# Optimization experiments

Hardware: AMD Instinct MI355X
Metric: run time of the kernel (lower is better)

The kernel has to match this reference:

```python
import jax, jax.numpy as jnp
import numpy as np
from jax import lax

B, N, K, M, NC = 64, 1024, 20, 256, 40  # clouds, points/cloud, knn k, fps points (ratio 0.25), classes
EPS = 1e-5


def setup_inputs() -> dict:
    key = jax.random.key(0)
    ks = jax.random.split(key, 6)
    w = lambda k, s: jax.random.normal(k, s, jnp.float32) * 0.05
    return {
        "pos": jax.random.normal(ks[0], (B * N, 3), jnp.float32),
        "w1": w(ks[1], (64, 3)), "b1": jnp.zeros(64, jnp.float32),
        "g1": jnp.ones(64, jnp.float32), "be1": jnp.zeros(64, jnp.float32),
        "w2": w(ks[2], (64, 64)), "b2": jnp.zeros(64, jnp.float32),
        "g2": jnp.ones(64, jnp.float32), "be2": jnp.zeros(64, jnp.float32),
        "w_nn1": w(ks[3], (512, 64)), "b_nn1": jnp.zeros(512, jnp.float32),
        "g_bn2": jnp.ones(512, jnp.float32), "be_bn2": jnp.zeros(512, jnp.float32),
        "w_nn4": w(ks[4], (NC, 512)), "b_nn4": jnp.zeros(NC, jnp.float32),
    }


def _knn_idx(p):  # p: [N,3] -> [N,K] neighbor indices, self excluded (loop=False)
    d = jnp.sum(p * p, -1)[:, None] + jnp.sum(p * p, -1)[None, :] - 2.0 * (p @ p.T)
    d = d.at[jnp.arange(N), jnp.arange(N)].set(jnp.inf)
    _, idx = lax.top_k(-d, K)
    return idx


def _fps_idx(p):  # p: [N,3] -> [M] farthest-point-sampling indices (deterministic start at 0)
    def step(carry, _):
        dist, last = carry
        d = jnp.sum((p - p[last]) ** 2, -1)
        dist = jnp.minimum(dist, d)
        nxt = jnp.argmax(dist).astype(jnp.int32)
        return (dist, nxt), nxt
    init = (jnp.full((N,), 1e38, jnp.float32), jnp.int32(0))
    _, idxs = lax.scan(step, init, None, length=M - 1)
    return jnp.concatenate([jnp.zeros((1,), jnp.int32), idxs])


def _bn(x, g, b, axes):  # batch-norm with batch statistics (training mode)
    m = jnp.mean(x, axes, keepdims=True)
    v = jnp.var(x, axes, keepdims=True)
    return (x - m) * lax.rsqrt(v + EPS) * g + b


def reference(pos, w1, b1, g1, be1, w2, b2, g2, be2,
              w_nn1, b_nn1, g_bn2, be_bn2, w_nn4, b_nn4):
    p = pos.reshape(B, N, 3)
    idx = jax.vmap(_knn_idx)(p)                     # [B,N,K]
    nbr = jax.vmap(lambda pb, ib: pb[ib])(p, idx)   # [B,N,K,3]
    rel = nbr - p[:, :, None, :]                    # edge features (relative positions)
    h = jax.nn.relu(jnp.einsum('bnkc,fc->bnkf', rel, w1) + b1)
    h = _bn(h, g1, be1, (0, 1, 2))
    h = jax.nn.relu(jnp.einsum('bnkf,gf->bnkg', h, w2) + b2)
    h = _bn(h, g2, be2, (0, 1, 2))
    feat = jnp.max(h, axis=2)                       # [B,N,64] edge-conv max aggregation
    fidx = jax.vmap(_fps_idx)(p)                    # [B,M]
    f = jnp.take_along_axis(feat, fidx[:, :, None], axis=1)  # [B,M,64]
    y = jnp.einsum('bmf,hf->bmh', f, w_nn1) + b_nn1  # [B,M,512]
    y = jnp.max(y, axis=1)                           # [B,512]
    y = jax.nn.relu(y)
    y = _bn(y, g_bn2, be_bn2, (0,))
    y = y @ w_nn4.T + b_nn4                          # [B,40]
    return jax.nn.log_softmax(y, axis=1)
```

## Files before the change

kernel.cpp:

```cpp
#include <hip/hip_runtime.h>
#include <hip/hip_bf16.h>
#include <cfloat>
#include <math.h>

#define BB 64
#define NN 1024
#define KNN 20
#define MM 256
#define CC 64
#define HH 512
#define NCLS 40
#define EPSF 1e-5f
#define CNT1 (BB*NN*KNN)

#define FPS_R1 101
#define FPS_R2 151

#define IDX_OFF    0
#define MAXH2_OFF  (IDX_OFF + BB*NN*KNN)
#define FIDX_OFF   (MAXH2_OFF + BB*NN*CC)
#define Y_OFF      (FIDX_OFF + BB*MM)
#define ACC_OFF    (Y_OFF + BB*HH)
#define W2T_OFF    (ACC_OFF + 256)
#define B2F_OFF    (W2T_OFF + CC*CC)
#define S2_OFF     (B2F_OFF + CC)
#define T2_OFF     (S2_OFF + CC)
#define S3_OFF     (T2_OFF + CC)
#define T3_OFF     (S3_OFF + HH)
#define FPSD_OFF   (T3_OFF + HH)
#define FPSC_OFF   (FPSD_OFF + BB*NN)

typedef __attribute__((ext_vector_type(8)))  short short8;
typedef __attribute__((ext_vector_type(16))) float f32x16;

static __device__ __forceinline__ unsigned short f2bf(float f) {
  unsigned u = __float_as_uint(f);
  unsigned r = (u + 0x7fffu + ((u >> 16) & 1u)) >> 16;
  return (unsigned short)r;
}

static __device__ __forceinline__ void fps_phase(
    const float* sx, const float* sy, const float* sz,
    float* fpsd, int* fpsc, int* fidxg, int b, int mStart, int mEnd) {
  int lane = threadIdx.x;
  float lx[16], ly[16], lz[16], dist[16];
#pragma unroll
  for (int q = 0; q < 16; ++q) {
    int j = q*64 + lane;
    lx[q] = sx[j]; ly[q] = sy[j]; lz[q] = sz[j];
  }
  int cur;
  if (mStart <= 1) {
#pragma unroll
    for (int q = 0; q < 16; ++q) dist[q] = 1e38f;
    if (lane == 0) fidxg[b*MM] = 0;
    cur = 0;
  } else {
#pragma unroll
    for (int q = 0; q < 16; ++q) dist[q] = fpsd[b*NN + q*64 + lane];
    cur = fpsc[b];
  }
  for (int m = mStart; m < mEnd; ++m) {
    float cpx = sx[cur], cpy = sy[cur], cpz = sz[cur];
#pragma unroll
    for (int q = 0; q < 16; ++q) {
      float dx = __fsub_rn(lx[q], cpx);
      float dy = __fsub_rn(ly[q], cpy);
      float dz = __fsub_rn(lz[q], cpz);
      float dd = __fadd_rn(__fadd_rn(__fmul_rn(dx,dx), __fmul_rn(dy,dy)), __fmul_rn(dz,dz));
      dist[q] = fminf(dist[q], dd);
    }
    float t8[8];
#pragma unroll
    for (int q = 0; q < 8; ++q) t8[q] = fmaxf(dist[q], dist[q + 8]);
#pragma unroll
    for (int q = 0; q < 4; ++q) t8[q] = fmaxf(t8[q], t8[q + 4]);
    float r = fmaxf(fmaxf(t8[0], t8[1]), fmaxf(t8[2], t8[3]));
#define FPS_VMAX_STEP(C) { \
    int tt = __builtin_amdgcn_update_dpp(__float_as_int(r), __float_as_int(r), (C), 0xf, 0xf, false); \
    r = fmaxf(r, __int_as_float(tt)); }
    FPS_VMAX_STEP(0x111)
    FPS_VMAX_STEP(0x112)
    FPS_VMAX_STEP(0x114)
    FPS_VMAX_STEP(0x118)
    FPS_VMAX_STEP(0x142)
    FPS_VMAX_STEP(0x143)
#undef FPS_VMAX_STEP
    float wmax = __int_as_float(__builtin_amdgcn_readlane(__float_as_int(r), 63));
    unsigned ci = 0xFFFFFFFFu;
#pragma unroll
    for (int q = 15; q >= 0; --q)
      if (dist[q] == wmax) ci = (unsigned)(q*64 + lane);
#define FPS_IMIN_STEP(C) { \
    unsigned tt = (unsigned)__builtin_amdgcn_update_dpp((int)ci, (int)ci, (C), 0xf, 0xf, false); \
    ci = (tt < ci) ? tt : ci; }
    FPS_IMIN_STEP(0x111)
    FPS_IMIN_STEP(0x112)
    FPS_IMIN_STEP(0x114)
    FPS_IMIN_STEP(0x118)
    FPS_IMIN_STEP(0x142)
    FPS_IMIN_STEP(0x143)
#undef FPS_IMIN_STEP
    cur = (int)(unsigned)__builtin_amdgcn_readlane((int)ci, 63);
    if (lane == 0) fidxg[b*MM + m] = cur;
  }
  if (mEnd < MM) {
#pragma unroll
    for (int q = 0; q < 16; ++q) fpsd[b*NN + q*64 + lane] = dist[q];
    if (lane == 0) fpsc[b] = cur;
  }
}

__global__ __launch_bounds__(256) void knn_fps_kernel(const float* __restrict__ pos,
                                                      int* __restrict__ idxg,
                                                      int* __restrict__ fidxg,
                                                      float* __restrict__ fpsd,
                                                      int* __restrict__ fpsc) {
  __shared__ float4 pj[NN];
  if (blockIdx.x >= BB) {
    int blk = blockIdx.x - BB;
    int b  = blk >> 5;
    int nb = blk & 31;
    const float* pb = pos + (size_t)b * NN * 3;
    for (int i = threadIdx.x; i < NN; i += 256) {
      float x = pb[i*3+0], y = pb[i*3+1], z = pb[i*3+2];
      pj[i] = make_float4(x, y, z, (x*x + y*y) + z*z);
    }
    __syncthreads();
    int lane = threadIdx.x & 63;
    int wv   = threadIdx.x >> 6;
    unsigned long long lmask_lt = (1ULL << lane) - 1ULL;

    for (int t = 0; t < 8; ++t) {
      int i = nb*32 + wv*8 + t;
      float4 pi = pj[i];
      unsigned u[16];
#pragma unroll
      for (int q = 0; q < 16; ++q) {
        int j = q*64 + lane;
        float4 pw = pj[j];
        float d = pi.w + pw.w - 2.0f*(pi.x*pw.x + pi.y*pw.y + pi.z*pw.z);
        unsigned bits = __float_as_uint(d);
        bits = (bits & 0x80000000u) ? ~bits : (bits | 0x80000000u);
        if (j == i) bits = 0xFFFFFFFFu;
        u[q] = bits;
      }
      unsigned lmin = u[0];
#pragma unroll
      for (int q = 1; q < 16; ++q) lmin = (u[q] < lmin) ? u[q] : lmin;
      unsigned rmin = lmin, rmax = lmin;
#define KNN_DPP_STEP(C) { \
      unsigned t1 = (unsigned)__builtin_amdgcn_update_dpp((int)rmin, (int)rmin, (C), 0xf, 0xf, false); \
      unsigned t2 = (unsigned)__builtin_amdgcn_update_dpp((int)rmax, (int)rmax, (C), 0xf, 0xf, false); \
      rmin = (t1 < rmin) ? t1 : rmin; rmax = (t2 > rmax) ? t2 : rmax; }
      KNN_DPP_STEP(0x111)
      KNN_DPP_STEP(0x112)
      KNN_DPP_STEP(0x114)
      KNN_DPP_STEP(0x118)
      KNN_DPP_STEP(0x142)
      KNN_DPP_STEP(0x143)
#undef KNN_DPP_STEP
      unsigned plo = ((unsigned)__builtin_amdgcn_readlane((int)rmin, 63)) >> 16;
      unsigned phi = ((unsigned)__builtin_amdgcn_readlane((int)rmax, 63)) >> 16;
      int cntHi = -1;
      while (plo < phi) {
        unsigned pmid = (plo + phi) >> 1;
        unsigned tmid = (pmid << 16) | 0xFFFFu;
        int cnt = 0;
#pragma unroll
        for (int q = 0; q < 16; ++q)
          cnt += (int)__popcll(__ballot(u[q] <= tmid));
        if (cnt >= KNN) { phi = pmid; cntHi = cnt; } else plo = pmid + 1;
      }
      unsigned tstar = (phi << 16) | 0xFFFFu;
      unsigned bbase = phi << 16;
      int* op = idxg + (size_t)(b*NN + i) * KNN;
      if (cntHi < 0) {
        cntHi = 0;
#pragma unroll
        for (int q = 0; q < 16; ++q)
          cntHi += (int)__popcll(__ballot(u[q] <= tstar));
      }
      if (cntHi == KNN) {
        int base = 0;
#pragma unroll
        for (int q = 0; q < 16; ++q) {
          bool pred = (u[q] <= tstar);
          unsigned long long mask = __ballot((int)pred);
          if (pred) op[base + (int)__popcll(mask & lmask_lt)] = q*64 + lane;
          base += (int)__popcll(mask);
        }
      } else {
        unsigned lo2 = bbase, hi2 = tstar;
        while (lo2 < hi2) {
          unsigned mid = lo2 + ((hi2 - lo2) >> 1);
          int cnt = 0;
#pragma unroll
          for (int q = 0; q < 16; ++q)
            cnt += (int)__popcll(__ballot(u[q] <= mid));
          if (cnt >= KNN) hi2 = mid; else lo2 = mid + 1;
        }
        unsigned xstar = lo2;
        int base = 0;
#pragma unroll
        for (int q = 0; q < 16; ++q) {
          bool pred = (u[q] < xstar);
          unsigned long long mask = __ballot((int)pred);
          if (pred) op[base + (int)__popcll(mask & lmask_lt)] = q*64 + lane;
          base += (int)__popcll(mask);
        }
        for (int q = 0; q < 16 && base < KNN; ++q) {
          bool pred = (u[q] == xstar);
          unsigned long long mask = __ballot((int)pred);
          if (pred) {
            int pos_ = base + (int)__popcll(mask & lmask_lt);
            if (pos_ < KNN) op[pos_] = q*64 + lane;
          }
          base += (int)__popcll(mask);
        }
      }
    }
  } else {
    int b = blockIdx.x;
    float* base = (float*)pj;
    float* sx = base; float* sy = base + NN; float* sz = base + 2*NN;
    const float* pb = pos + (size_t)b * NN * 3;
    for (int i = threadIdx.x; i < NN; i += 256) {
      sx[i] = pb[i*3+0]; sy[i] = pb[i*3+1]; sz[i] = pb[i*3+2];
    }
    __syncthreads();
    if (threadIdx.x >= 64) return;
    fps_phase(sx, sy, sz, fpsd, fpsc, fidxg, b, 1, FPS_R1);
  }
}

__global__ __launch_bounds__(256) void stats1_kernel(const float* __restrict__ pos,
    const int* __restrict__ idxg, const float* __restrict__ w1,
    const float* __restrict__ b1, float* __restrict__ acc,
    int* __restrict__ fidxg, float* __restrict__ fpsd, int* __restrict__ fpsc) {
  __shared__ float px[NN], py[NN], pz[NN];
  __shared__ float relx[4][KNN], rely[4][KNN], relz[4][KNN];
  __shared__ float red[4][CC];
  if (blockIdx.x < BB) {
    int b = blockIdx.x;
    const float* pb = pos + (size_t)b*NN*3;
    for (int i = threadIdx.x; i < NN; i += 256) {
      px[i] = pb[i*3+0]; py[i] = pb[i*3+1]; pz[i] = pb[i*3+2];
    }
    __syncthreads();
    if (threadIdx.x >= 64) return;
    fps_phase(px, py, pz, fpsd, fpsc, fidxg, b, FPS_R1, FPS_R2);
    return;
  }
  int blk = blockIdx.x - BB;
  int b = blk >> 4;
  int nb = blk & 15;
  const float* pb = pos + (size_t)b*NN*3;
  for (int i = threadIdx.x; i < NN; i += 256) {
    px[i] = pb[i*3+0]; py[i] = pb[i*3+1]; pz[i] = pb[i*3+2];
  }
  int c = threadIdx.x & 63, w = threadIdx.x >> 6;
  float w1x = w1[c*3+0], w1y = w1[c*3+1], w1z = w1[c*3+2], b1c = b1[c];
  float s = 0.f, ss = 0.f;
  __syncthreads();
  for (int it = 0; it < 16; ++it) {
    int n0 = nb*64 + it*4;
    if (threadIdx.x < 80) {
      int wv = threadIdx.x / KNN, k = threadIdx.x % KNN;
      int n = n0 + wv;
      int j = idxg[(size_t)(b*NN + n)*KNN + k];
      relx[wv][k] = px[j] - px[n];
      rely[wv][k] = py[j] - py[n];
      relz[wv][k] = pz[j] - pz[n];
    }
    __syncthreads();
#pragma unroll
    for (int k = 0; k < KNN; ++k) {
      float h = fmaxf(relx[w][k]*w1x + rely[w][k]*w1y + relz[w][k]*w1z + b1c, 0.f);
      s += h; ss += h*h;
    }
    __syncthreads();
  }
  red[w][c] = s; __syncthreads();
  if (w == 0) atomicAdd(&acc[c], red[0][c]+red[1][c]+red[2][c]+red[3][c]);
  __syncthreads();
  red[w][c] = ss; __syncthreads();
  if (w == 0) atomicAdd(&acc[64+c], red[0][c]+red[1][c]+red[2][c]+red[3][c]);
}

__global__ void fold1_kernel(const float* __restrict__ acc, const float* __restrict__ g1,
    const float* __restrict__ be1, const float* __restrict__ w2, const float* __restrict__ b2,
    unsigned short* __restrict__ w2bf, float* __restrict__ b2f) {
  __shared__ float s1[CC], t1[CC];
  int tid = threadIdx.x;
  if (tid < CC) {
    float cnt = (float)CNT1;
    float m = acc[tid] / cnt;
    float v = acc[64+tid] / cnt - m*m;
    float sc = g1[tid] * rsqrtf(v + EPSF);
    s1[tid] = sc; t1[tid] = be1[tid] - m*sc;
  }
  __syncthreads();
  int frag = tid >> 6;
  int lane = tid & 63;
  int nt = frag >> 2, ks = frag & 3;
  int cout = nt*32 + (lane & 31);
  int cin0 = ks*16 + (lane >> 5)*8;
  for (int j = 0; j < 8; ++j) {
    int cin = cin0 + j;
    w2bf[((size_t)frag*64 + lane)*8 + j] = f2bf(w2[cout*CC + cin] * s1[cin]);
  }
  if (tid < CC) {
    float accb = b2[tid];
    for (int ci = 0; ci < CC; ++ci) accb += t1[ci]*w2[tid*CC + ci];
    b2f[tid] = accb;
  }
}

__global__ __launch_bounds__(256, 4) void conv2_kernel(const float* __restrict__ pos,
    const int* __restrict__ idxg, const float* __restrict__ w1, const float* __restrict__ b1,
    const unsigned short* __restrict__ w2bf, const float* __restrict__ b2fg,
    float* __restrict__ maxh2, float* __restrict__ acc2,
    int* __restrict__ fidxg, float* __restrict__ fpsd, int* __restrict__ fpsc) {
  __shared__ float px[NN], py[NN], pz[NN];
  __shared__ float4 relw[4][KNN];
  __shared__ __align__(16) unsigned short h1s[4][2112];
  __shared__ float redbuf[4][2*CC];
  if (blockIdx.x < BB) {
    int b = blockIdx.x;
    const float* pb = pos + (size_t)b*NN*3;
    for (int i = threadIdx.x; i < NN; i += 256) {
      px[i] = pb[i*3+0]; py[i] = pb[i*3+1]; pz[i] = pb[i*3+2];
    }
    __syncthreads();
    if (threadIdx.x >= 64) return;
    fps_phase(px, py, pz, fpsd, fpsc, fidxg, b, FPS_R2, MM);
    return;
  }
  int blk = blockIdx.x - BB;
  int b = blk >> 4;
  int nb = blk & 15;
  const float* pb = pos + (size_t)b*NN*3;
  for (int i = threadIdx.x; i < NN; i += 256) {
    px[i] = pb[i*3+0]; py[i] = pb[i*3+1]; pz[i] = pb[i*3+2];
  }
  int lane = threadIdx.x & 63, w = threadIdx.x >> 6;
  int half = lane >> 5, l31 = lane & 31;
  short8 Bf[2][4];
#pragma unroll
  for (int nt = 0; nt < 2; ++nt)
#pragma unroll
    for (int ks = 0; ks < 4; ++ks)
      Bf[nt][ks] = *(const short8*)&w2bf[((size_t)(nt*4+ks)*64 + lane)*8];
  float b2o0 = b2fg[l31], b2o1 = b2fg[32 + l31];
  float w1x = w1[lane*3+0], w1y = w1[lane*3+1], w1z = w1[lane*3+2], b1c = b1[lane];
  unsigned short* hw = h1s[w];
  {
    short8 zz = {0,0,0,0,0,0,0,0};
    for (int z = lane; z < 96; z += 64) {
      int g = z / 12, r = 20 + z % 12;
      *(short8*)&hw[g*264 + r*8] = zz;
    }
  }
  float sA = 0.f, ssA = 0.f, sB = 0.f, ssB = 0.f;
  __syncthreads();
  for (int t = 0; t < 16; ++t) {
    int n = nb*64 + w*16 + t;
    if (lane < KNN) {
      int j = idxg[(size_t)(b*NN + n)*KNN + lane];
      relw[w][lane] = make_float4(px[j]-px[n], py[j]-py[n], pz[j]-pz[n], 0.f);
    }
    int gbase = (lane >> 3)*264 + (lane & 7);
#pragma unroll
    for (int k = 0; k < KNN; ++k) {
      float4 r4 = relw[w][k];
      float h = fmaxf(fmaf(r4.x, w1x, fmaf(r4.y, w1y, fmaf(r4.z, w1z, b1c))), 0.f);
      hw[gbase + k*8] = f2bf(h);
    }
    f32x16 acc0 = {}; f32x16 acc1 = {};
#pragma unroll
    for (int ks = 0; ks < 4; ++ks) {
      short8 A = *(const short8*)&hw[(ks*2 + half)*264 + l31*8];
      acc0 = __builtin_amdgcn_mfma_f32_32x32x16_bf16(A, Bf[0][ks], acc0, 0, 0, 0);
      acc1 = __builtin_amdgcn_mfma_f32_32x32x16_bf16(A, Bf[1][ks], acc1, 0, 0, 0);
    }
    float mx0 = 0.f, mx1 = 0.f;
#pragma unroll
    for (int reg = 0; reg < 8; ++reg) {
      float v0 = fmaxf(acc0[reg] + b2o0, 0.f);
      float v1 = fmaxf(acc1[reg] + b2o1, 0.f);
      sA += v0; ssA += v0*v0; sB += v1; ssB += v1*v1;
      mx0 = fmaxf(mx0, v0); mx1 = fmaxf(mx1, v1);
    }
    if (half == 0) {
#pragma unroll
      for (int reg = 8; reg < 12; ++reg) {
        float v0 = fmaxf(acc0[reg] + b2o0, 0.f);
        float v1 = fmaxf(acc1[reg] + b2o1, 0.f);
        sA += v0; ssA += v0*v0; sB += v1; ssB += v1*v1;
        mx0 = fmaxf(mx0, v0); mx1 = fmaxf(mx1, v1);
      }
    }
    mx0 = fmaxf(mx0, __shfl_xor(mx0, 32, 64));
    mx1 = fmaxf(mx1, __shfl_xor(mx1, 32, 64));
    if (half == 0) {
      float* mp = maxh2 + (size_t)(b*NN + n)*CC;
      mp[l31] = mx0; mp[32 + l31] = mx1;
    }
  }
  sA += __shfl_xor(sA, 32, 64); ssA += __shfl_xor(ssA, 32, 64);
  sB += __shfl_xor(sB, 32, 64); ssB += __shfl_xor(ssB, 32, 64);
  if (half == 0) { redbuf[w][l31] = sA; redbuf[w][32 + l31] = sB; }
  __syncthreads();
  if (w == 0) atomicAdd(&acc2[lane], redbuf[0][lane]+redbuf[1][lane]+redbuf[2][lane]+redbuf[3][lane]);
  __syncthreads();
  if (half == 0) { redbuf[w][l31] = ssA; redbuf[w][32 + l31] = ssB; }
  __syncthreads();
  if (w == 0) atomicAdd(&acc2[64+lane], redbuf[0][lane]+redbuf[1][lane]+redbuf[2][lane]+redbuf[3][lane]);
}

__global__ void fold2_kernel(const float* __restrict__ acc2, const float* __restrict__ g2,
    const float* __restrict__ be2, float* __restrict__ s2, float* __restrict__ t2) {
  int c = threadIdx.x;
  float cnt = (float)CNT1;
  float m = acc2[c]/cnt;
  float v = acc2[64+c]/cnt - m*m;
  float sc = g2[c]*rsqrtf(v+EPSF);
  s2[c] = sc;
  t2[c] = be2[c] - m*sc;
}

__global__ __launch_bounds__(256) void head_kernel(const float* __restrict__ maxh2,
    const int* __restrict__ fidxg, const float* __restrict__ s2g, const float* __restrict__ t2g,
    const float* __restrict__ wnn1, const float* __restrict__ bnn1, float* __restrict__ Y) {
  int b = blockIdx.x >> 2;
  int hc = blockIdx.x & 3;
  __shared__ __align__(16) float ftile[128][CC];
  __shared__ float red2[4][128];
  int hl = threadIdx.x & 63, mseg = threadIdx.x >> 6;
  int hA = hc*128 + hl, hB = hA + 64;
  float4 wva[16], wvb[16];
  const float4* wrA = (const float4*)(wnn1 + (size_t)hA*CC);
  const float4* wrB = (const float4*)(wnn1 + (size_t)hB*CC);
#pragma unroll
  for (int q = 0; q < 16; ++q) { wva[q] = wrA[q]; wvb[q] = wrB[q]; }
  float bestA = -FLT_MAX, bestB = -FLT_MAX;
  const int* fb = fidxg + b*MM;
  for (int chunk = 0; chunk < 2; ++chunk) {
    {
      int row = threadIdx.x & 127, chal = threadIdx.x >> 7;
      int fi = fb[chunk*128 + row];
      const float* src = maxh2 + (size_t)(b*NN + fi)*CC;
      for (int ci = chal*32; ci < chal*32+32; ++ci)
        ftile[row][ci] = s2g[ci]*src[ci] + t2g[ci];
    }
    __syncthreads();
    for (int m = mseg*32; m < mseg*32+32; ++m) {
      float accA = 0.f, accB = 0.f;
#pragma unroll
      for (int cq = 0; cq < 16; ++cq) {
        float4 f = *((const float4*)&ftile[m][cq*4]);
        accA = fmaf(f.x, wva[cq].x, accA);
        accA = fmaf(f.y, wva[cq].y, accA);
        accA = fmaf(f.z, wva[cq].z, accA);
        accA = fmaf(f.w, wva[cq].w, accA);
        accB = fmaf(f.x, wvb[cq].x, accB);
        accB = fmaf(f.y, wvb[cq].y, accB);
        accB = fmaf(f.z, wvb[cq].z, accB);
        accB = fmaf(f.w, wvb[cq].w, accB);
      }
      bestA = fmaxf(bestA, accA);
      bestB = fmaxf(bestB, accB);
    }
    __syncthreads();
  }
  red2[mseg][hl] = bestA;
  red2[mseg][64 + hl] = bestB;
  __syncthreads();
  if (threadIdx.x < 128) {
    int hh = hc*128 + threadIdx.x;
    float v = fmaxf(fmaxf(red2[0][threadIdx.x], red2[1][threadIdx.x]),
                    fmaxf(red2[2][threadIdx.x], red2[3][threadIdx.x])) + bnn1[hh];
    Y[(size_t)b*HH + hh] = fmaxf(v, 0.f);
  }
}

__global__ void bn3_kernel(const float* __restrict__ Y, const float* __restrict__ g,
    const float* __restrict__ be, float* __restrict__ s3, float* __restrict__ t3) {
  int h = blockIdx.x*256 + threadIdx.x;
  float s = 0.f;
  for (int b = 0; b < BB; ++b) s += Y[(size_t)b*HH + h];
  float m = s / (float)BB;
  float v = 0.f;
  for (int b = 0; b < BB; ++b) { float d = Y[(size_t)b*HH + h] - m; v += d*d; }
  v /= (float)BB;
  float sc = g[h] * rsqrtf(v + EPSF);
  s3[h] = sc; t3[h] = be[h] - m*sc;
}

__global__ __launch_bounds__(256) void logits_kernel(const float* __restrict__ Y,
    const float* __restrict__ s3, const float* __restrict__ t3,
    const float* __restrict__ w4, const float* __restrict__ b4, float* __restrict__ out) {
  int b = blockIdx.x;
  __shared__ float ybn[HH];
  __shared__ float lg[NCLS];
  __shared__ float lse;
  for (int hh = threadIdx.x; hh < HH; hh += 256)
    ybn[hh] = Y[(size_t)b*HH + hh]*s3[hh] + t3[hh];
  __syncthreads();
  if (threadIdx.x < NCLS) {
    int j = threadIdx.x;
    float acc = b4[j];
    const float* wr = w4 + (size_t)j*HH;
    for (int ci = 0; ci < HH; ++ci) acc = fmaf(ybn[ci], wr[ci], acc);
    lg[j] = acc;
  }
  __syncthreads();
  if (threadIdx.x == 0) {
    float mx = -FLT_MAX;
    for (int j = 0; j < NCLS; ++j) mx = fmaxf(mx, lg[j]);
    float s = 0.f;
    for (int j = 0; j < NCLS; ++j) s += expf(lg[j] - mx);
    lse = mx + logf(s);
  }
  __syncthreads();
  if (threadIdx.x < NCLS) out[b*NCLS + threadIdx.x] = lg[threadIdx.x] - lse;
}

extern "C" void kernel_launch(void* const* d_in, const int* in_sizes, int n_in,
                              void* d_out, int out_size, void* d_ws, size_t ws_size,
                              hipStream_t stream) {
  const float* pos  = (const float*)d_in[0];
  const float* w1   = (const float*)d_in[1];
  const float* b1   = (const float*)d_in[2];
  const float* g1   = (const float*)d_in[3];
  const float* be1  = (const float*)d_in[4];
  const float* w2   = (const float*)d_in[5];
  const float* b2   = (const float*)d_in[6];
  const float* g2   = (const float*)d_in[7];
  const float* be2  = (const float*)d_in[8];
  const float* wnn1 = (const float*)d_in[9];
  const float* bnn1 = (const float*)d_in[10];
  const float* gbn2 = (const float*)d_in[11];
  const float* bebn2= (const float*)d_in[12];
  const float* wnn4 = (const float*)d_in[13];
  const float* bnn4 = (const float*)d_in[14];
  float* ws = (float*)d_ws;
  int*   idxg  = (int*)(ws + IDX_OFF);
  float* maxh2 = ws + MAXH2_OFF;
  int*   fidxg = (int*)(ws + FIDX_OFF);
  float* Y     = ws + Y_OFF;
  float* acc1  = ws + ACC_OFF;
  float* acc2  = ws + ACC_OFF + 128;
  unsigned short* w2bf = (unsigned short*)(ws + W2T_OFF);
  float* b2f   = ws + B2F_OFF;
  float* s2    = ws + S2_OFF;
  float* t2    = ws + T2_OFF;
  float* s3    = ws + S3_OFF;
  float* t3    = ws + T3_OFF;
  float* fpsd  = ws + FPSD_OFF;
  int*   fpsc  = (int*)(ws + FPSC_OFF);
  float* outp  = (float*)d_out;

  hipMemsetAsync((void*)(ws + ACC_OFF), 0, 256*sizeof(float), stream);
  knn_fps_kernel<<<BB + BB*32, 256, 0, stream>>>(pos, idxg, fidxg, fpsd, fpsc);
  stats1_kernel<<<BB + BB*16, 256, 0, stream>>>(pos, idxg, w1, b1, acc1, fidxg, fpsd, fpsc);
  fold1_kernel<<<1, 512, 0, stream>>>(acc1, g1, be1, w2, b2, w2bf, b2f);
  conv2_kernel<<<BB + BB*16, 256, 0, stream>>>(pos, idxg, w1, b1, w2bf, b2f, maxh2, acc2, fidxg, fpsd, fpsc);
  fold2_kernel<<<1, 64, 0, stream>>>(acc2, g2, be2, s2, t2);
  head_kernel<<<BB*4, 256, 0, stream>>>(maxh2, fidxg, s2, t2, wnn1, bnn1, Y);
  bn3_kernel<<<2, 256, 0, stream>>>(Y, gbn2, bebn2, s3, t3);
  logits_kernel<<<BB, 256, 0, stream>>>(Y, s3, t3, wnn4, bnn4, outp);
}
```

Before: 371.4 us.

## Process two KNN query points per wave iteration and rebalance FPS split

The KNN selection loop now handles two query points at once. Their distance computation, DPP reductions and radix-threshold binary searches are interleaved so the serial ballot/popcount chains overlap for instruction-level parallelism. Lane prefix counts now use mbcnt instead of a mask-and-popcount, and the FPS phase boundaries are moved so more iterations run inside the concurrent KNN kernel. The interleaved search runs until both points converge, so one point may do wasted iterations, and register pressure rises.

```diff
diff --git a/kernel.cpp b/kernel.cpp
--- a/kernel.cpp
+++ b/kernel.cpp
@@ -13,8 +13,8 @@
 #define EPSF 1e-5f
 #define CNT1 (BB*NN*KNN)
 
-#define FPS_R1 101
-#define FPS_R2 151
+#define FPS_R1 131
+#define FPS_R2 176
 
 #define IDX_OFF    0
 #define MAXH2_OFF  (IDX_OFF + BB*NN*KNN)
@@ -37,6 +37,55 @@
   unsigned u = __float_as_uint(f);
   unsigned r = (u + 0x7fffu + ((u >> 16) & 1u)) >> 16;
   return (unsigned short)r;
+}
+
+static __device__ __forceinline__ int mbcnt64(unsigned long long m) {
+  return (int)__builtin_amdgcn_mbcnt_hi((unsigned)(m >> 32),
+           __builtin_amdgcn_mbcnt_lo((unsigned)m, 0));
+}
+
+static __device__ __forceinline__ void knn_emit_generic(const unsigned* u, unsigned phi,
+                                                        int cntHi, int* op, int lane) {
+  unsigned tstar = (phi << 16) | 0xFFFFu;
+  unsigned bbase = phi << 16;
+  if (cntHi == KNN) {
+    int base = 0;
+#pragma unroll
+    for (int q = 0; q < 16; ++q) {
+      bool pred = (u[q] <= tstar);
+      unsigned long long mask = __ballot((int)pred);
+      if (pred) op[base + mbcnt64(mask)] = q*64 + lane;
+      base += (int)__popcll(mask);
+    }
+  } else {
+    unsigned lo2 = bbase, hi2 = tstar;
+    while (lo2 < hi2) {
+      unsigned mid = lo2 + ((hi2 - lo2) >> 1);
+      int cnt = 0;
+#pragma unroll
+      for (int q = 0; q < 16; ++q)
+        cnt += (int)__popcll(__ballot(u[q] <= mid));
+      if (cnt >= KNN) hi2 = mid; else lo2 = mid + 1;
+    }
+    unsigned xstar = lo2;
+    int base = 0;
+#pragma unroll
+    for (int q = 0; q < 16; ++q) {
+      bool pred = (u[q] < xstar);
+      unsigned long long mask = __ballot((int)pred);
+      if (pred) op[base + mbcnt64(mask)] = q*64 + lane;
+      base += (int)__popcll(mask);
+    }
+    for (int q = 0; q < 16 && base < KNN; ++q) {
+      bool pred = (u[q] == xstar);
+      unsigned long long mask = __ballot((int)pred);
+      if (pred) {
+        int pos_ = base + mbcnt64(mask);
+        if (pos_ < KNN) op[pos_] = q*64 + lane;
+      }
+      base += (int)__popcll(mask);
+    }
+  }
 }
 
 static __device__ __forceinline__ void fps_phase(
@@ -129,30 +178,42 @@
     __syncthreads();
     int lane = threadIdx.x & 63;
     int wv   = threadIdx.x >> 6;
-    unsigned long long lmask_lt = (1ULL << lane) - 1ULL;
-
-    for (int t = 0; t < 8; ++t) {
-      int i = nb*32 + wv*8 + t;
-      float4 pi = pj[i];
-      unsigned u[16];
+
+    for (int t = 0; t < 4; ++t) {
+      int iA = nb*32 + wv*8 + 2*t;
+      int iB = iA + 1;
+      float4 piA = pj[iA];
+      float4 piB = pj[iB];
+      unsigned uA[16], uB[16];
 #pragma unroll
       for (int q = 0; q < 16; ++q) {
         int j = q*64 + lane;
         float4 pw = pj[j];
-        float d = pi.w + pw.w - 2.0f*(pi.x*pw.x + pi.y*pw.y + pi.z*pw.z);
-        unsigned bits = __float_as_uint(d);
-        bits = (bits & 0x80000000u) ? ~bits : (bits | 0x80000000u);
-        if (j == i) bits = 0xFFFFFFFFu;
-        u[q] = bits;
-      }
-      unsigned lmin = u[0];
-#pragma unroll
-      for (int q = 1; q < 16; ++q) lmin = (u[q] < lmin) ? u[q] : lmin;
-      unsigned rmin = lmin, rmax = lmin;
+        float dA = piA.w + pw.w - 2.0f*(piA.x*pw.x + piA.y*pw.y + piA.z*pw.z);
+        float dB = piB.w + pw.w - 2.0f*(piB.x*pw.x + piB.y*pw.y + piB.z*pw.z);
+        unsigned ba = __float_as_uint(dA);
+        ba = (ba & 0x80000000u) ? ~ba : (ba | 0x80000000u);
+        if (j == iA) ba = 0xFFFFFFFFu;
+        uA[q] = ba;
+        unsigned bb2 = __float_as_uint(dB);
+        bb2 = (bb2 & 0x80000000u) ? ~bb2 : (bb2 | 0x80000000u);
+        if (j == iB) bb2 = 0xFFFFFFFFu;
+        uB[q] = bb2;
+      }
+      unsigned lminA = uA[0], lminB = uB[0];
+#pragma unroll
+      for (int q = 1; q < 16; ++q) {
+        lminA = (uA[q] < lminA) ? uA[q] : lminA;
+        lminB = (uB[q] < lminB) ? uB[q] : lminB;
+      }
+      unsigned rminA = lminA, rmaxA = lminA, rminB = lminB, rmaxB = lminB;
 #define KNN_DPP_STEP(C) { \
-      unsigned t1 = (unsigned)__builtin_amdgcn_update_dpp((int)rmin, (int)rmin, (C), 0xf, 0xf, false); \
-      unsigned t2 = (unsigned)__builtin_amdgcn_update_dpp((int)rmax, (int)rmax, (C), 0xf, 0xf, false); \
-      rmin = (t1 < rmin) ? t1 : rmin; rmax = (t2 > rmax) ? t2 : rmax; }
+      unsigned t1 = (unsigned)__builtin_amdgcn_update_dpp((int)rminA, (int)rminA, (C), 0xf, 0xf, false); \
+      unsigned t2 = (unsigned)__builtin_amdgcn_update_dpp((int)rmaxA, (int)rmaxA, (C), 0xf, 0xf, false); \
+      unsigned t3 = (unsigned)__builtin_amdgcn_update_dpp((int)rminB, (int)rminB, (C), 0xf, 0xf, false); \
+      unsigned t4 = (unsigned)__builtin_amdgcn_update_dpp((int)rmaxB, (int)rmaxB, (C), 0xf, 0xf, false); \
+      rminA = (t1 < rminA) ? t1 : rminA; rmaxA = (t2 > rmaxA) ? t2 : rmaxA; \
+      rminB = (t3 < rminB) ? t3 : rminB; rmaxB = (t4 > rmaxB) ? t4 : rmaxB; }
       KNN_DPP_STEP(0x111)
       KNN_DPP_STEP(0x112)
       KNN_DPP_STEP(0x114)
@@ -160,64 +221,53 @@
       KNN_DPP_STEP(0x142)
       KNN_DPP_STEP(0x143)
 #undef KNN_DPP_STEP
-      unsigned plo = ((unsigned)__builtin_amdgcn_readlane((int)rmin, 63)) >> 16;
-      unsigned phi = ((unsigned)__builtin_amdgcn_readlane((int)rmax, 63)) >> 16;
-      int cntHi = -1;
-      while (plo < phi) {
-        unsigned pmid = (plo + phi) >> 1;
-        unsigned tmid = (pmid << 16) | 0xFFFFu;
-        int cnt = 0;
-#pragma unroll
-        for (int q = 0; q < 16; ++q)
-          cnt += (int)__popcll(__ballot(u[q] <= tmid));
-        if (cnt >= KNN) { phi = pmid; cntHi = cnt; } else plo = pmid + 1;
-      }
-      unsigned tstar = (phi << 16) | 0xFFFFu;
-      unsigned bbase = phi << 16;
-      int* op = idxg + (size_t)(b*NN + i) * KNN;
-      if (cntHi < 0) {
-        cntHi = 0;
-#pragma unroll
-        for (int q = 0; q < 16; ++q)
-          cntHi += (int)__popcll(__ballot(u[q] <= tstar));
-      }
-      if (cntHi == KNN) {
-        int base = 0;
+      unsigned ploA = ((unsigned)__builtin_amdgcn_readlane((int)rminA, 63)) >> 16;
+      unsigned phiA = ((unsigned)__builtin_amdgcn_readlane((int)rmaxA, 63)) >> 16;
+      unsigned ploB = ((unsigned)__builtin_amdgcn_readlane((int)rminB, 63)) >> 16;
+      unsigned phiB = ((unsigned)__builtin_amdgcn_readlane((int)rmaxB, 63)) >> 16;
+      int cntHiA = -1, cntHiB = -1;
+      while (ploA < phiA || ploB < phiB) {
+        unsigned pmA = (ploA + phiA) >> 1, pmB = (ploB + phiB) >> 1;
+        unsigned tA = (pmA << 16) | 0xFFFFu, tB = (pmB << 16) | 0xFFFFu;
+        int cA = 0, cB = 0;
 #pragma unroll
         for (int q = 0; q < 16; ++q) {
-          bool pred = (u[q] <= tstar);
-          unsigned long long mask = __ballot((int)pred);
-          if (pred) op[base + (int)__popcll(mask & lmask_lt)] = q*64 + lane;
-          base += (int)__popcll(mask);
+          cA += (int)__popcll(__ballot(uA[q] <= tA));
+          cB += (int)__popcll(__ballot(uB[q] <= tB));
+        }
+        if (ploA < phiA) { if (cA >= KNN) { phiA = pmA; cntHiA = cA; } else ploA = pmA + 1; }
+        if (ploB < phiB) { if (cB >= KNN) { phiB = pmB; cntHiB = cB; } else ploB = pmB + 1; }
+      }
+      if (cntHiA < 0 || cntHiB < 0) {
+        unsigned tsA = (phiA << 16) | 0xFFFFu, tsB = (phiB << 16) | 0xFFFFu;
+        int cA = 0, cB = 0;
+#pragma unroll
+        for (int q = 0; q < 16; ++q) {
+          cA += (int)__popcll(__ballot(uA[q] <= tsA));
+          cB += (int)__popcll(__ballot(uB[q] <= tsB));
+        }
+        if (cntHiA < 0) cntHiA = cA;
+        if (cntHiB < 0) cntHiB = cB;
+      }
+      int* opA = idxg + (size_t)(b*NN + iA) * KNN;
+      int* opB = idxg + (size_t)(b*NN + iB) * KNN;
+      if (cntHiA == KNN && cntHiB == KNN) {
+        unsigned tsA = (phiA << 16) | 0xFFFFu, tsB = (phiB << 16) | 0xFFFFu;
+        int baseA = 0, baseB = 0;
+#pragma unroll
+        for (int q = 0; q < 16; ++q) {
+          bool pA = (uA[q] <= tsA);
+          unsigned long long mA = __ballot((int)pA);
+          bool pB = (uB[q] <= tsB);
+          unsigned long long mB = __ballot((int)pB);
+          if (pA) opA[baseA + mbcnt64(mA)] = q*64 + lane;
+          if (pB) opB[baseB + mbcnt64(mB)] = q*64 + lane;
+          baseA += (int)__popcll(mA);
+          baseB += (int)__popcll(mB);
         }
       } else {
-        unsigned lo2 = bbase, hi2 = tstar;
-        while (lo2 < hi2) {
-          unsigned mid = lo2 + ((hi2 - lo2) >> 1);
-          int cnt = 0;
-#pragma unroll
-          for (int q = 0; q < 16; ++q)
-            cnt += (int)__popcll(__ballot(u[q] <= mid));
-          if (cnt >= KNN) hi2 = mid; else lo2 = mid + 1;
-        }
-        unsigned xstar = lo2;
-        int base = 0;
-#pragma unroll
-        for (int q = 0; q < 16; ++q) {
-          bool pred = (u[q] < xstar);
-          unsigned long long mask = __ballot((int)pred);
-          if (pred) op[base + (int)__popcll(mask & lmask_lt)] = q*64 + lane;
-          base += (int)__popcll(mask);
-        }
-        for (int q = 0; q < 16 && base < KNN; ++q) {
-          bool pred = (u[q] == xstar);
-          unsigned long long mask = __ballot((int)pred);
-          if (pred) {
-            int pos_ = base + (int)__popcll(mask & lmask_lt);
-            if (pos_ < KNN) op[pos_] = q*64 + lane;
-          }
-          base += (int)__popcll(mask);
-        }
+        knn_emit_generic(uA, phiA, cntHiA, opA, lane);
+        knn_emit_generic(uB, phiB, cntHiB, opB, lane);
       }
     }
   } else {
```

Measured after the change: 409.1 us. 1.1x slower.

## Fuse BN fold kernels into head and logits kernels, rebalance FPS phase split

Applied to the files above, without the earlier changes.

Removes the separate fold2 and bn3 launches. Each head block now recomputes the BN2 scale and shift into shared memory, and each logits block recomputes the BN3 batch statistics redundantly. This removes two tiny kernel launches and their serialization gaps. The FPS phase boundaries (how the sampling steps are split across the knn, stats and conv kernels) also move later, shifting work between the fused kernels. The cost is redundant per-block reduction work: every one of the 64 logits blocks rereads all of Y.

```diff
diff --git a/kernel.cpp b/kernel.cpp
--- a/kernel.cpp
+++ b/kernel.cpp
@@ -13,8 +13,8 @@
 #define EPSF 1e-5f
 #define CNT1 (BB*NN*KNN)
 
-#define FPS_R1 101
-#define FPS_R2 151
+#define FPS_R1 131
+#define FPS_R2 176
 
 #define IDX_OFF    0
 #define MAXH2_OFF  (IDX_OFF + BB*NN*KNN)
@@ -23,11 +23,7 @@
 #define ACC_OFF    (Y_OFF + BB*HH)
 #define W2T_OFF    (ACC_OFF + 256)
 #define B2F_OFF    (W2T_OFF + CC*CC)
-#define S2_OFF     (B2F_OFF + CC)
-#define T2_OFF     (S2_OFF + CC)
-#define S3_OFF     (T2_OFF + CC)
-#define T3_OFF     (S3_OFF + HH)
-#define FPSD_OFF   (T3_OFF + HH)
+#define FPSD_OFF   (B2F_OFF + CC)
 #define FPSC_OFF   (FPSD_OFF + BB*NN)
 
 typedef __attribute__((ext_vector_type(8)))  short short8;
@@ -419,24 +415,24 @@
   if (w == 0) atomicAdd(&acc2[64+lane], redbuf[0][lane]+redbuf[1][lane]+redbuf[2][lane]+redbuf[3][lane]);
 }
 
-__global__ void fold2_kernel(const float* __restrict__ acc2, const float* __restrict__ g2,
-    const float* __restrict__ be2, float* __restrict__ s2, float* __restrict__ t2) {
-  int c = threadIdx.x;
-  float cnt = (float)CNT1;
-  float m = acc2[c]/cnt;
-  float v = acc2[64+c]/cnt - m*m;
-  float sc = g2[c]*rsqrtf(v+EPSF);
-  s2[c] = sc;
-  t2[c] = be2[c] - m*sc;
-}
-
 __global__ __launch_bounds__(256) void head_kernel(const float* __restrict__ maxh2,
-    const int* __restrict__ fidxg, const float* __restrict__ s2g, const float* __restrict__ t2g,
+    const int* __restrict__ fidxg, const float* __restrict__ acc2,
+    const float* __restrict__ g2, const float* __restrict__ be2,
     const float* __restrict__ wnn1, const float* __restrict__ bnn1, float* __restrict__ Y) {
   int b = blockIdx.x >> 2;
   int hc = blockIdx.x & 3;
   __shared__ __align__(16) float ftile[128][CC];
   __shared__ float red2[4][128];
+  __shared__ float s2s[CC], t2s[CC];
+  if (threadIdx.x < CC) {
+    int c = threadIdx.x;
+    float cnt = (float)CNT1;
+    float m = acc2[c]/cnt;
+    float v = acc2[64+c]/cnt - m*m;
+    float sc = g2[c]*rsqrtf(v+EPSF);
+    s2s[c] = sc;
+    t2s[c] = be2[c] - m*sc;
+  }
   int hl = threadIdx.x & 63, mseg = threadIdx.x >> 6;
   int hA = hc*128 + hl, hB = hA + 64;
   float4 wva[16], wvb[16];
@@ -446,13 +442,14 @@
   for (int q = 0; q < 16; ++q) { wva[q] = wrA[q]; wvb[q] = wrB[q]; }
   float bestA = -FLT_MAX, bestB = -FLT_MAX;
   const int* fb = fidxg + b*MM;
+  __syncthreads();
   for (int chunk = 0; chunk < 2; ++chunk) {
     {
       int row = threadIdx.x & 127, chal = threadIdx.x >> 7;
       int fi = fb[chunk*128 + row];
       const float* src = maxh2 + (size_t)(b*NN + fi)*CC;
       for (int ci = chal*32; ci < chal*32+32; ++ci)
-        ftile[row][ci] = s2g[ci]*src[ci] + t2g[ci];
+        ftile[row][ci] = s2s[ci]*src[ci] + t2s[ci];
     }
     __syncthreads();
     for (int m = mseg*32; m < mseg*32+32; ++m) {
@@ -485,28 +482,27 @@
   }
 }
 
-__global__ void bn3_kernel(const float* __restrict__ Y, const float* __restrict__ g,
-    const float* __restrict__ be, float* __restrict__ s3, float* __restrict__ t3) {
-  int h = blockIdx.x*256 + threadIdx.x;
-  float s = 0.f;
-  for (int b = 0; b < BB; ++b) s += Y[(size_t)b*HH + h];
-  float m = s / (float)BB;
-  float v = 0.f;
-  for (int b = 0; b < BB; ++b) { float d = Y[(size_t)b*HH + h] - m; v += d*d; }
-  v /= (float)BB;
-  float sc = g[h] * rsqrtf(v + EPSF);
-  s3[h] = sc; t3[h] = be[h] - m*sc;
-}
-
 __global__ __launch_bounds__(256) void logits_kernel(const float* __restrict__ Y,
-    const float* __restrict__ s3, const float* __restrict__ t3,
+    const float* __restrict__ g3, const float* __restrict__ be3,
     const float* __restrict__ w4, const float* __restrict__ b4, float* __restrict__ out) {
   int b = blockIdx.x;
   __shared__ float ybn[HH];
+  __shared__ float s3s[HH], t3s[HH];
   __shared__ float lg[NCLS];
   __shared__ float lse;
+  for (int h = threadIdx.x; h < HH; h += 256) {
+    float s = 0.f;
+    for (int bb = 0; bb < BB; ++bb) s += Y[(size_t)bb*HH + h];
+    float m = s / (float)BB;
+    float v = 0.f;
+    for (int bb = 0; bb < BB; ++bb) { float d = Y[(size_t)bb*HH + h] - m; v += d*d; }
+    v /= (float)BB;
+    float sc = g3[h] * rsqrtf(v + EPSF);
+    s3s[h] = sc; t3s[h] = be3[h] - m*sc;
+  }
+  __syncthreads();
   for (int hh = threadIdx.x; hh < HH; hh += 256)
-    ybn[hh] = Y[(size_t)b*HH + hh]*s3[hh] + t3[hh];
+    ybn[hh] = Y[(size_t)b*HH + hh]*s3s[hh] + t3s[hh];
   __syncthreads();
   if (threadIdx.x < NCLS) {
     int j = threadIdx.x;
@@ -554,10 +550,6 @@
   float* acc2  = ws + ACC_OFF + 128;
   unsigned short* w2bf = (unsigned short*)(ws + W2T_OFF);
   float* b2f   = ws + B2F_OFF;
-  float* s2    = ws + S2_OFF;
-  float* t2    = ws + T2_OFF;
-  float* s3    = ws + S3_OFF;
-  float* t3    = ws + T3_OFF;
   float* fpsd  = ws + FPSD_OFF;
   int*   fpsc  = (int*)(ws + FPSC_OFF);
   float* outp  = (float*)d_out;
@@ -567,8 +559,6 @@
   stats1_kernel<<<BB + BB*16, 256, 0, stream>>>(pos, idxg, w1, b1, acc1, fidxg, fpsd, fpsc);
   fold1_kernel<<<1, 512, 0, stream>>>(acc1, g1, be1, w2, b2, w2bf, b2f);
   conv2_kernel<<<BB + BB*16, 256, 0, stream>>>(pos, idxg, w1, b1, w2bf, b2f, maxh2, acc2, fidxg, fpsd, fpsc);
-  fold2_kernel<<<1, 64, 0, stream>>>(acc2, g2, be2, s2, t2);
-  head_kernel<<<BB*4, 256, 0, stream>>>(maxh2, fidxg, s2, t2, wnn1, bnn1, Y);
-  bn3_kernel<<<2, 256, 0, stream>>>(Y, gbn2, bebn2, s3, t3);
-  logits_kernel<<<BB, 256, 0, stream>>>(Y, s3, t3, wnn4, bnn4, outp);
-}
+  head_kernel<<<BB*4, 256, 0, stream>>>(maxh2, fidxg, acc2, g2, be2, wnn1, bnn1, Y);
+  logits_kernel<<<BB, 256, 0, stream>>>(Y, gbn2, bebn2, wnn4, bnn4, outp);
+}
```

After: 352.6 us. 5.0% less time.
